# Kernel tuning notes

Hardware: AMD Instinct MI355X
Metric: run time of the kernel (lower is better)

## Reference

```python
import jax, jax.numpy as jnp
import numpy as np

B, T, C = 4, 8192, 1024
H, D = 16, 64  # n_head, head_dim


def setup_inputs() -> dict:
    key = jax.random.key(0)
    ks = jax.random.split(key, 9)
    s = 1.0 / np.sqrt(C)
    return {
        "x": jax.random.normal(ks[0], (B, T, C), jnp.float32),
        "Wq": jax.random.uniform(ks[1], (C, C), jnp.float32, -s, s),
        "bq": jax.random.uniform(ks[2], (C,), jnp.float32, -s, s),
        "Wk": jax.random.uniform(ks[3], (C, C), jnp.float32, -s, s),
        "bk": jax.random.uniform(ks[4], (C,), jnp.float32, -s, s),
        "Wv": jax.random.uniform(ks[5], (C, C), jnp.float32, -s, s),
        "bv": jax.random.uniform(ks[6], (C,), jnp.float32, -s, s),
        "Wp": jax.random.uniform(ks[7], (C, C), jnp.float32, -s, s),
        "bp": jax.random.uniform(ks[8], (C,), jnp.float32, -s, s),
    }


def _heads(t):
    # (B,T,C) -> (B,H,T,D)
    return t.reshape(B, T, H, D).transpose(0, 2, 1, 3)


def reference(x, Wq, bq, Wk, bk, Wv, bv, Wp, bp):
    q = _heads(x @ Wq.T + bq)
    k = _heads(x @ Wk.T + bk)
    v = _heads(x @ Wv.T + bv)
    # attn_type='l1': softmax q,k over feature dim; L1 normalizer
    q = jax.nn.softmax(q, axis=-1)
    k = jax.nn.softmax(k, axis=-1)
    k_sum = k.sum(axis=-2, keepdims=True)               # (B,H,1,D)
    D_inv = 1.0 / (q * k_sum).sum(axis=-1, keepdims=True)  # (B,H,T,1)
    context = jnp.einsum('bhtd,bhte->bhde', k, v)       # (B,H,D,D)
    out = jnp.einsum('bhtd,bhde->bhte', q, context) * D_inv + q
    out = out.transpose(0, 2, 1, 3).reshape(B, T, C)
    return out @ Wp.T + bp
```

## Files before the change

### kernel.cpp

```cpp
#include <hip/hip_runtime.h>
#include <hip/hip_bf16.h>
#include <stdint.h>


#define BT    32768
#define CDIM  1024

using bf16 = __hip_bfloat16;
typedef short  short8   __attribute__((ext_vector_type(8)));
typedef short  short4_t __attribute__((ext_vector_type(4)));
typedef unsigned short ushort4_t __attribute__((ext_vector_type(4)));
typedef float  floatx4  __attribute__((ext_vector_type(4)));

__device__ __forceinline__ float bfbits2f(unsigned short u) {
    union { unsigned int i; float f; } c; c.i = ((unsigned int)u) << 16; return c.f;
}

__device__ __forceinline__ void gld_lds16(const void* g, void* lds) {
    __builtin_amdgcn_global_load_lds(
        (const __attribute__((address_space(1))) uint32_t*)g,
        (__attribute__((address_space(3))) uint32_t*)lds,
        16, 0, 0);
}

__global__ void zero_kernel(float* __restrict__ p) {
    p[(size_t)blockIdx.x * 256 + threadIdx.x] = 0.0f;
}

__global__ void cvt_kernel(const float* __restrict__ x,
                           const float* __restrict__ Wq, const float* __restrict__ Wk,
                           const float* __restrict__ Wv, const float* __restrict__ Wp,
                           bf16* __restrict__ xb, bf16* __restrict__ Wb) {
    const int XF4 = (BT * CDIM) / 4;
    int i = blockIdx.x * 256 + threadIdx.x;
    const float* src; bf16* dst; int off;
    if (i < XF4) { src = x; dst = xb; off = i; }
    else {
        int i2 = i - XF4;
        int wi = i2 >> 18;
        off = i2 & 0x3FFFF;
        src = (wi == 0) ? Wq : (wi == 1) ? Wk : (wi == 2) ? Wv : Wp;
        dst = Wb + (size_t)wi * 1048576;
    }
    float4 f = ((const float4*)src)[off];
    union { bf16 h[4]; short4_t v; } u;
    u.h[0] = __float2bfloat16(f.x); u.h[1] = __float2bfloat16(f.y);
    u.h[2] = __float2bfloat16(f.z); u.h[3] = __float2bfloat16(f.w);
    *(short4_t*)(dst + (size_t)off * 4) = u.v;
}


__device__ __forceinline__ short8 frag_ld(const bf16* hb, int r, int s4q) {
    return *(const short8*)(hb + r * 64 + (((s4q) ^ (r & 7)) << 3));
}

__device__ __forceinline__ void stage_half(const bf16* g, bf16* l, int tid) {
    int ln = tid & 63, w = tid >> 6;
    int r = w * 8 + (ln >> 3);
    int c = ((ln & 7) ^ (ln >> 3)) << 3;
    gld_lds16(g + (size_t)r * CDIM + c, l + w * 512);
    gld_lds16(g + (size_t)(r + 64) * CDIM + c, l + 4096 + w * 512);
}

#define MFMA16(a, b, c) __builtin_amdgcn_mfma_f32_16x16x32_bf16(a, b, c, 0, 0, 0)
#define VMW(n) asm volatile("s_waitcnt vmcnt(" #n ")" ::: "memory")
#define VM_NONE

__device__ __forceinline__ void pipe256(const bf16* __restrict__ Ab,
                                        const bf16* __restrict__ Bb,
                                        bf16* ldsA, bf16* ldsB,
                                        int tid, floatx4 acc[8][4]) {
    const int lane = tid & 63;
    const int wv = tid >> 6;
    const int quad = lane >> 4, l15 = lane & 15;
    const int wm = wv >> 2, wn = wv & 3;
    const int rA0 = wm * 64 + l15;
    const int rB0 = (wn & 1) * 64 + l15;
    const bf16* ldsBh = ldsB + (wn >> 1) * 8192;
    short8 bfr[4][2];

#define STAGE_A(b, h, kt) stage_half(Ab + (size_t)((h) * 128) * CDIM + (kt) * 64, \
                                     ldsA + (b) * 16384 + (h) * 8192, tid)
#define STAGE_B(b, h, kt) stage_half(Bb + (size_t)((h) * 128) * CDIM + (kt) * 64, \
                                     ldsB + (b) * 16384 + (h) * 8192, tid)

#define QPHASE(BUF, QA, MM, LOADB, STG, VMC) do {                              \
    const bf16* aH_ = ldsA + (BUF) * 16384 + (QA) * 8192;                      \
    short8 a00_ = frag_ld(aH_, rA0 + (MM) * 32,      quad);                    \
    short8 a01_ = frag_ld(aH_, rA0 + (MM) * 32,      4 + quad);                \
    short8 a10_ = frag_ld(aH_, rA0 + (MM) * 32 + 16, quad);                    \
    short8 a11_ = frag_ld(aH_, rA0 + (MM) * 32 + 16, 4 + quad);                \
    if (LOADB) {                                                               \
        const bf16* bH_ = ldsBh + (BUF) * 16384;                               \
        _Pragma("unroll")                                                      \
        for (int j = 0; j < 4; ++j) {                                          \
            bfr[j][0] = frag_ld(bH_, rB0 + j * 16, quad);                      \
            bfr[j][1] = frag_ld(bH_, rB0 + j * 16, 4 + quad);                  \
        }                                                                      \
    }                                                                          \
    STG; VMC;                                                                  \
    __builtin_amdgcn_s_barrier();                                              \
    asm volatile("s_waitcnt lgkmcnt(0)" ::: "memory");                         \
    __builtin_amdgcn_s_setprio(1);                                             \
    _Pragma("unroll")                                                          \
    for (int j = 0; j < 4; ++j) {                                              \
        acc[(QA)*4+(MM)*2  ][j] = MFMA16(a00_, bfr[j][0], acc[(QA)*4+(MM)*2  ][j]); \
        acc[(QA)*4+(MM)*2  ][j] = MFMA16(a01_, bfr[j][1], acc[(QA)*4+(MM)*2  ][j]); \
        acc[(QA)*4+(MM)*2+1][j] = MFMA16(a10_, bfr[j][0], acc[(QA)*4+(MM)*2+1][j]); \
        acc[(QA)*4+(MM)*2+1][j] = MFMA16(a11_, bfr[j][1], acc[(QA)*4+(MM)*2+1][j]); \
    }                                                                          \
    __builtin_amdgcn_s_setprio(0);                                             \
    __builtin_amdgcn_s_barrier();                                              \
} while (0)

    STAGE_B(0, 0, 0); STAGE_B(0, 1, 0); STAGE_A(0, 0, 0); STAGE_A(0, 1, 0);
    STAGE_B(1, 0, 1); STAGE_B(1, 1, 1); STAGE_A(1, 0, 1);
    VMW(8);
    __builtin_amdgcn_s_barrier();

    #pragma unroll 1
    for (int i = 0; i < 7; ++i) {
        int t = 2 * i;
        QPHASE(0, 0, 0, 1, STAGE_A(1, 1, t + 1), VM_NONE);
        QPHASE(0, 0, 1, 0, STAGE_B(0, 0, t + 2), VMW(10));
        QPHASE(0, 1, 0, 0, STAGE_B(0, 1, t + 2), VM_NONE);
        QPHASE(0, 1, 1, 0, STAGE_A(0, 0, t + 2), VMW(8));
        QPHASE(1, 0, 0, 1, STAGE_A(0, 1, t + 2), VM_NONE);
        QPHASE(1, 0, 1, 0, STAGE_B(1, 0, t + 3), VMW(10));
        QPHASE(1, 1, 0, 0, STAGE_B(1, 1, t + 3), VM_NONE);
        QPHASE(1, 1, 1, 0, STAGE_A(1, 0, t + 3), VMW(8));
    }
    QPHASE(0, 0, 0, 1, STAGE_A(1, 1, 15), VM_NONE);
    QPHASE(0, 0, 1, 0, VM_NONE, VMW(8));
    QPHASE(0, 1, 0, 0, VM_NONE, VM_NONE);
    QPHASE(0, 1, 1, 0, VM_NONE, VMW(2));
    QPHASE(1, 0, 0, 1, VM_NONE, VM_NONE);
    QPHASE(1, 0, 1, 0, VM_NONE, VMW(0));
    QPHASE(1, 1, 0, 0, VM_NONE, VM_NONE);
    QPHASE(1, 1, 1, 0, VM_NONE, VM_NONE);

#undef QPHASE
#undef STAGE_A
#undef STAGE_B
}

__global__ __launch_bounds__(512, 2)
void gemm_qkv(const bf16* __restrict__ A, const bf16* __restrict__ Bw,
              const float* __restrict__ bq, const float* __restrict__ bk,
              const float* __restrict__ bv,
              bf16* __restrict__ qb, bf16* __restrict__ kb, bf16* __restrict__ vb) {
    __shared__ bf16 ldsA[32768];
    __shared__ bf16 ldsB[32768];
    int tid = threadIdx.x;
    int bid = blockIdx.x;
    int swz = (bid & 7) * 192 + (bid >> 3);
    int bn = swz % 12, bm = swz / 12;

    floatx4 acc[8][4] = {};
    pipe256(A + (size_t)bm * 256 * CDIM, Bw + (size_t)bn * 256 * CDIM,
            ldsA, ldsB, tid, acc);

    int lane = tid & 63, wv = tid >> 6, quad = lane >> 4, l15 = lane & 15;
    int wm = wv >> 2, wn = wv & 3;
    int n_abs = bn * 256 + wn * 64;
    bf16* dst; const float* biasp; int ncol0; bool smax;
    if (n_abs < 1024)      { dst = qb; biasp = bq; ncol0 = n_abs;        smax = true;  }
    else if (n_abs < 2048) { dst = kb; biasp = bk; ncol0 = n_abs - 1024; smax = true;  }
    else                   { dst = vb; biasp = bv; ncol0 = n_abs - 2048; smax = false; }
    float bias4[4];
    #pragma unroll
    for (int j = 0; j < 4; ++j) bias4[j] = biasp[ncol0 + j * 16 + l15];
    size_t row0 = (size_t)bm * 256 + wm * 64;

    #pragma unroll
    for (int i = 0; i < 8; ++i) {
        #pragma unroll
        for (int r = 0; r < 4; ++r) {
            float vals[4];
            #pragma unroll
            for (int j = 0; j < 4; ++j) vals[j] = acc[i][j][r] + bias4[j];
            if (smax) {
                float mx = fmaxf(fmaxf(vals[0], vals[1]), fmaxf(vals[2], vals[3]));
                #pragma unroll
                for (int d = 1; d < 16; d <<= 1) mx = fmaxf(mx, __shfl_xor(mx, d));
                float s = 0.f;
                #pragma unroll
                for (int j = 0; j < 4; ++j) { vals[j] = __expf(vals[j] - mx); s += vals[j]; }
                #pragma unroll
                for (int d = 1; d < 16; d <<= 1) s += __shfl_xor(s, d);
                float rinv = 1.0f / s;
                #pragma unroll
                for (int j = 0; j < 4; ++j) vals[j] *= rinv;
            }
            size_t row = row0 + ((i >> 2) * 128) + ((i & 3) * 16) + quad * 4 + r;
            #pragma unroll
            for (int j = 0; j < 4; ++j)
                dst[row * 1024 + ncol0 + j * 16 + l15] = __float2bfloat16(vals[j]);
        }
    }
}

__global__ __launch_bounds__(512, 2)
void gemm_out(const bf16* __restrict__ A, const bf16* __restrict__ Bw,
              const float* __restrict__ bp, float* __restrict__ outp) {
    __shared__ bf16 ldsA[32768];
    __shared__ bf16 ldsB[32768];
    int tid = threadIdx.x;
    int bid = blockIdx.x;
    int swz = (bid & 7) * 64 + (bid >> 3);
    int bn = swz & 3, bm = swz >> 2;

    floatx4 acc[8][4] = {};
    pipe256(A + (size_t)bm * 256 * CDIM, Bw + (size_t)bn * 256 * CDIM,
            ldsA, ldsB, tid, acc);

    int lane = tid & 63, wv = tid >> 6, quad = lane >> 4, l15 = lane & 15;
    int wm = wv >> 2, wn = wv & 3;
    int gcol0 = bn * 256 + wn * 64;
    float bias4[4];
    #pragma unroll
    for (int j = 0; j < 4; ++j) bias4[j] = bp[gcol0 + j * 16 + l15];
    size_t row0 = (size_t)bm * 256 + wm * 64;

    #pragma unroll
    for (int i = 0; i < 8; ++i) {
        #pragma unroll
        for (int r = 0; r < 4; ++r) {
            size_t row = row0 + ((i >> 2) * 128) + ((i & 3) * 16) + quad * 4 + r;
            #pragma unroll
            for (int j = 0; j < 4; ++j)
                outp[row * 1024 + gcol0 + j * 16 + l15] = acc[i][j][r] + bias4[j];
        }
    }
}

__global__ __launch_bounds__(256)
void ctx_kernel(const bf16* __restrict__ kbuf, const bf16* __restrict__ vbuf,
                float* __restrict__ ctx, float* __restrict__ ksum) {
    int bid = blockIdx.x;
    int head = bid >> 4, chunk = bid & 15;
    int b = head >> 4, h = head & 15;
    size_t rowbase = (size_t)b * 8192 + (size_t)chunk * 512;
    int coff = h * 64;
    __shared__ unsigned short kT[4096];
    __shared__ unsigned short vT[4096];
    __shared__ float ksum_s[64];
    int tid = threadIdx.x, lane = tid & 63, wv = tid >> 6;
    int quad = lane >> 4, l15 = lane & 15;
    int c8 = tid & 7, trow = tid >> 3;
    if (tid < 64) ksum_s[tid] = 0.f;

    float kacc[8] = {0.f, 0.f, 0.f, 0.f, 0.f, 0.f, 0.f, 0.f};
    floatx4 acc4[4] = {};

    size_t g0 = (rowbase + trow) * 1024 + coff + c8 * 8;
    short8 pk0 = *(const short8*)(kbuf + g0);
    short8 pk1 = *(const short8*)(kbuf + g0 + 32 * 1024);
    short8 pv0 = *(const short8*)(vbuf + g0);
    short8 pv1 = *(const short8*)(vbuf + g0 + 32 * 1024);

    int tb0 = trow >> 3;
    for (int st = 0; st < 8; ++st) {
        __syncthreads();
        #pragma unroll
        for (int j = 0; j < 8; ++j) {
            int d = c8 * 8 + j;
            int base = d * 64 + (trow & 7);
            int sw0 = (tb0 ^ j ^ c8) << 3;
            int sw1 = ((tb0 + 4) ^ j ^ c8) << 3;
            unsigned short ku0 = (unsigned short)((short*)&pk0)[j];
            unsigned short ku1 = (unsigned short)((short*)&pk1)[j];
            kT[base + sw0] = ku0;
            kT[base + sw1] = ku1;
            vT[base + sw0] = (unsigned short)((short*)&pv0)[j];
            vT[base + sw1] = (unsigned short)((short*)&pv1)[j];
            kacc[j] += bfbits2f(ku0) + bfbits2f(ku1);
        }
        __syncthreads();
        if (st < 7) {
            size_t g = g0 + (size_t)(st + 1) * 64 * 1024;
            pk0 = *(const short8*)(kbuf + g);
            pk1 = *(const short8*)(kbuf + g + 32 * 1024);
            pv0 = *(const short8*)(vbuf + g);
            pv1 = *(const short8*)(vbuf + g + 32 * 1024);
        }
        #pragma unroll
        for (int ks = 0; ks < 2; ++ks) {
            int dA = wv * 16 + l15;
            int blkA = (ks * 4 + quad) ^ (dA & 7) ^ (dA >> 3);
            short8 aF = *(const short8*)&kT[dA * 64 + (blkA << 3)];
            #pragma unroll
            for (int n = 0; n < 4; ++n) {
                int eB = n * 16 + l15;
                int blkB = (ks * 4 + quad) ^ (eB & 7) ^ (eB >> 3);
                short8 bF = *(const short8*)&vT[eB * 64 + (blkB << 3)];
                acc4[n] = MFMA16(aF, bF, acc4[n]);
            }
        }
    }

    #pragma unroll
    for (int j = 0; j < 8; ++j) {
        float v = kacc[j];
        v += __shfl_xor(v, 8); v += __shfl_xor(v, 16); v += __shfl_xor(v, 32);
        if (lane < 8) atomicAdd(&ksum_s[lane * 8 + j], v);
    }
    float* cptr = ctx + (size_t)head * 4096;
    #pragma unroll
    for (int n = 0; n < 4; ++n)
        #pragma unroll
        for (int rr = 0; rr < 4; ++rr) {
            int d = wv * 16 + quad * 4 + rr;
            int e = n * 16 + l15;
            atomicAdd(&cptr[d * 64 + e], acc4[n][rr]);
        }
    __syncthreads();
    if (tid < 64) atomicAdd(&ksum[head * 64 + tid], ksum_s[tid]);
}

#define QS 72
__global__ __launch_bounds__(256)
void attn_kernel(const bf16* __restrict__ qbuf, const float* __restrict__ ctx,
                 const float* __restrict__ ksum, bf16* __restrict__ ab) {
    int bid = blockIdx.x;
    int head = bid >> 7, tb = bid & 127;
    int b = head >> 4, h = head & 15;
    size_t row0 = (size_t)b * 8192 + (size_t)tb * 64;
    int coff = h * 64;
    __shared__ bf16 qs[64 * QS];
    __shared__ bf16 cts[64 * QS];
    __shared__ float ksums[64];
    __shared__ float dinv[64];
    int tid = threadIdx.x, lane = tid & 63, wv = tid >> 6;

    {
        int lrow = tid >> 2, lpart = tid & 3;
        size_t g = (row0 + lrow) * 1024 + coff + lpart * 16;
        short8 q0 = *(const short8*)(qbuf + g);
        short8 q1 = *(const short8*)(qbuf + g + 8);
        *(short8*)&qs[lrow * QS + lpart * 16]     = q0;
        *(short8*)&qs[lrow * QS + lpart * 16 + 8] = q1;
    }
    {
        const float* cp = ctx + (size_t)head * 4096;
        #pragma unroll
        for (int it = 0; it < 4; ++it) {
            int fi = it * 256 + tid;
            int d = fi >> 4, e0 = (fi & 15) * 4;
            float4 f = ((const float4*)cp)[fi];
            cts[(e0 + 0) * QS + d] = __float2bfloat16(f.x);
            cts[(e0 + 1) * QS + d] = __float2bfloat16(f.y);
            cts[(e0 + 2) * QS + d] = __float2bfloat16(f.z);
            cts[(e0 + 3) * QS + d] = __float2bfloat16(f.w);
        }
    }
    if (tid < 64) ksums[tid] = ksum[head * 64 + tid];
    __syncthreads();

    {
        int t = tid >> 2, dg = tid & 3;
        float p = 0.f;
        #pragma unroll
        for (int j = 0; j < 16; ++j)
            p = fmaf(__bfloat162float(qs[t * QS + dg * 16 + j]), ksums[dg * 16 + j], p);
        p += __shfl_xor(p, 1);
        p += __shfl_xor(p, 2);
        if (dg == 0) dinv[t] = 1.0f / p;
    }
    __syncthreads();

    int quad = lane >> 4, l15 = lane & 15;
    int trow0 = wv * 16;
    short8 aF0 = *(const short8*)&qs[(trow0 + l15) * QS + quad * 8];
    short8 aF1 = *(const short8*)&qs[(trow0 + l15) * QS + 32 + quad * 8];
    floatx4 acc[4] = {};
    #pragma unroll
    for (int ni = 0; ni < 4; ++ni) {
        short8 b0 = *(const short8*)&cts[(ni * 16 + l15) * QS + quad * 8];
        short8 b1 = *(const short8*)&cts[(ni * 16 + l15) * QS + 32 + quad * 8];
        acc[ni] = __builtin_amdgcn_mfma_f32_16x16x32_bf16(aF0, b0, acc[ni], 0, 0, 0);
        acc[ni] = __builtin_amdgcn_mfma_f32_16x16x32_bf16(aF1, b1, acc[ni], 0, 0, 0);
    }
    float dv[4];
    #pragma unroll
    for (int r = 0; r < 4; ++r) dv[r] = dinv[trow0 + quad * 4 + r];
    #pragma unroll
    for (int ni = 0; ni < 4; ++ni) {
        #pragma unroll
        for (int r = 0; r < 4; ++r) {
            int row = trow0 + quad * 4 + r;
            int col = ni * 16 + l15;
            float val = acc[ni][r] * dv[r] + __bfloat162float(qs[row * QS + col]);
            ab[(row0 + row) * 1024 + coff + col] = __float2bfloat16(val);
        }
    }
}

extern "C" void kernel_launch(void* const* d_in, const int* in_sizes, int n_in,
                              void* d_out, int out_size, void* d_ws, size_t ws_size,
                              hipStream_t stream) {
    const float* x  = (const float*)d_in[0];
    const float* Wq = (const float*)d_in[1];
    const float* bq = (const float*)d_in[2];
    const float* Wk = (const float*)d_in[3];
    const float* bk = (const float*)d_in[4];
    const float* Wv = (const float*)d_in[5];
    const float* bv = (const float*)d_in[6];
    const float* Wp = (const float*)d_in[7];
    const float* bp = (const float*)d_in[8];
    float* outp = (float*)d_out;

    char* ws = (char*)d_ws;
    bf16*  xb   = (bf16*)(ws);
    bf16*  Wb   = (bf16*)(ws + 67108864);
    bf16*  qb   = (bf16*)(ws + 75497472);
    bf16*  kb   = (bf16*)(ws + 142606336);
    bf16*  vb   = (bf16*)(ws + 209715200);
    float* ctx  = (float*)(ws + 276824064);
    float* ksum = (float*)(ws + 277872640);
    bf16*  ab   = (bf16*)(ws);

    zero_kernel<<<1040, 256, 0, stream>>>(ctx);
    cvt_kernel<<<36864, 256, 0, stream>>>(x, Wq, Wk, Wv, Wp, xb, Wb);
    gemm_qkv<<<1536, 512, 0, stream>>>(xb, Wb, bq, bk, bv, qb, kb, vb);
    ctx_kernel<<<1024, 256, 0, stream>>>(kb, vb, ctx, ksum);
    attn_kernel<<<8192, 256, 0, stream>>>(qb, ctx, ksum, ab);
    gemm_out<<<512, 512, 0, stream>>>(ab, Wb + (size_t)3072 * 1024, bp, outp);
}
```

Baseline: 646.7 us.

## Fuse zeroing into conversion kernel, loop attn over row tiles, nontemporal output stores

Merges the ctx/ksum zeroing kernel into the fp32→bf16 conversion kernel, which now uses a grid-stride loop with 4096 blocks instead of 36864. The attention kernel now processes four 64-row tiles per block, loading the per-head context matrix once per block and prefetching the next q tile into registers while it computes on double-buffered LDS. The output GEMM writes its final fp32 results with nontemporal stores. The aim is to cut launch count, per-block context reload and conversion work, and cache pollution from the output writes, at the cost of fewer blocks for latency hiding in the attention kernel.

```diff
diff --git a/kernel.cpp b/kernel.cpp
--- a/kernel.cpp
+++ b/kernel.cpp
@@ -23,30 +23,36 @@
         16, 0, 0);
 }
 
-__global__ void zero_kernel(float* __restrict__ p) {
-    p[(size_t)blockIdx.x * 256 + threadIdx.x] = 0.0f;
-}
-
-__global__ void cvt_kernel(const float* __restrict__ x,
-                           const float* __restrict__ Wq, const float* __restrict__ Wk,
-                           const float* __restrict__ Wv, const float* __restrict__ Wp,
-                           bf16* __restrict__ xb, bf16* __restrict__ Wb) {
+__global__ __launch_bounds__(256)
+void prep_kernel(const float* __restrict__ x,
+                 const float* __restrict__ Wq, const float* __restrict__ Wk,
+                 const float* __restrict__ Wv, const float* __restrict__ Wp,
+                 bf16* __restrict__ xb, bf16* __restrict__ Wb,
+                 float* __restrict__ zp) {
     const int XF4 = (BT * CDIM) / 4;
-    int i = blockIdx.x * 256 + threadIdx.x;
-    const float* src; bf16* dst; int off;
-    if (i < XF4) { src = x; dst = xb; off = i; }
-    else {
-        int i2 = i - XF4;
-        int wi = i2 >> 18;
-        off = i2 & 0x3FFFF;
-        src = (wi == 0) ? Wq : (wi == 1) ? Wk : (wi == 2) ? Wv : Wp;
-        dst = Wb + (size_t)wi * 1048576;
-    }
-    float4 f = ((const float4*)src)[off];
-    union { bf16 h[4]; short4_t v; } u;
-    u.h[0] = __float2bfloat16(f.x); u.h[1] = __float2bfloat16(f.y);
-    u.h[2] = __float2bfloat16(f.z); u.h[3] = __float2bfloat16(f.w);
-    *(short4_t*)(dst + (size_t)off * 4) = u.v;
+    const int TOT = XF4 + 4 * 262144;
+    int t0 = blockIdx.x * 256 + threadIdx.x;
+    if (t0 < 66560) {
+        float4 z = {0.f, 0.f, 0.f, 0.f};
+        ((float4*)zp)[t0] = z;
+    }
+    #pragma unroll 1
+    for (int i = t0; i < TOT; i += 1048576) {
+        const float* src; bf16* dst; int off;
+        if (i < XF4) { src = x; dst = xb; off = i; }
+        else {
+            int i2 = i - XF4;
+            int wi = i2 >> 18;
+            off = i2 & 0x3FFFF;
+            src = (wi == 0) ? Wq : (wi == 1) ? Wk : (wi == 2) ? Wv : Wp;
+            dst = Wb + (size_t)wi * 1048576;
+        }
+        float4 f = ((const float4*)src)[off];
+        union { bf16 h[4]; short4_t v; } u;
+        u.h[0] = __float2bfloat16(f.x); u.h[1] = __float2bfloat16(f.y);
+        u.h[2] = __float2bfloat16(f.z); u.h[3] = __float2bfloat16(f.w);
+        *(short4_t*)(dst + (size_t)off * 4) = u.v;
+    }
 }
 
 
@@ -229,7 +235,8 @@
             size_t row = row0 + ((i >> 2) * 128) + ((i & 3) * 16) + quad * 4 + r;
             #pragma unroll
             for (int j = 0; j < 4; ++j)
-                outp[row * 1024 + gcol0 + j * 16 + l15] = acc[i][j][r] + bias4[j];
+                __builtin_nontemporal_store(acc[i][j][r] + bias4[j],
+                    &outp[row * 1024 + gcol0 + j * 16 + l15]);
         }
     }
 }
@@ -323,24 +330,18 @@
 void attn_kernel(const bf16* __restrict__ qbuf, const float* __restrict__ ctx,
                  const float* __restrict__ ksum, bf16* __restrict__ ab) {
     int bid = blockIdx.x;
-    int head = bid >> 7, tb = bid & 127;
+    int head = bid >> 5, grp = bid & 31;
     int b = head >> 4, h = head & 15;
-    size_t row0 = (size_t)b * 8192 + (size_t)tb * 64;
     int coff = h * 64;
-    __shared__ bf16 qs[64 * QS];
+    __shared__ bf16 qs[2][64 * QS];
     __shared__ bf16 cts[64 * QS];
     __shared__ float ksums[64];
     __shared__ float dinv[64];
     int tid = threadIdx.x, lane = tid & 63, wv = tid >> 6;
-
-    {
-        int lrow = tid >> 2, lpart = tid & 3;
-        size_t g = (row0 + lrow) * 1024 + coff + lpart * 16;
-        short8 q0 = *(const short8*)(qbuf + g);
-        short8 q1 = *(const short8*)(qbuf + g + 8);
-        *(short8*)&qs[lrow * QS + lpart * 16]     = q0;
-        *(short8*)&qs[lrow * QS + lpart * 16 + 8] = q1;
-    }
+    int lrow = tid >> 2, lpart = tid & 3;
+    int quad = lane >> 4, l15 = lane & 15;
+    int trow0 = wv * 16;
+
     {
         const float* cp = ctx + (size_t)head * 4096;
         #pragma unroll
@@ -355,43 +356,58 @@
         }
     }
     if (tid < 64) ksums[tid] = ksum[head * 64 + tid];
-    __syncthreads();
-
-    {
-        int t = tid >> 2, dg = tid & 3;
-        float p = 0.f;
-        #pragma unroll
-        for (int j = 0; j < 16; ++j)
-            p = fmaf(__bfloat162float(qs[t * QS + dg * 16 + j]), ksums[dg * 16 + j], p);
-        p += __shfl_xor(p, 1);
-        p += __shfl_xor(p, 2);
-        if (dg == 0) dinv[t] = 1.0f / p;
-    }
-    __syncthreads();
-
-    int quad = lane >> 4, l15 = lane & 15;
-    int trow0 = wv * 16;
-    short8 aF0 = *(const short8*)&qs[(trow0 + l15) * QS + quad * 8];
-    short8 aF1 = *(const short8*)&qs[(trow0 + l15) * QS + 32 + quad * 8];
-    floatx4 acc[4] = {};
-    #pragma unroll
-    for (int ni = 0; ni < 4; ++ni) {
-        short8 b0 = *(const short8*)&cts[(ni * 16 + l15) * QS + quad * 8];
-        short8 b1 = *(const short8*)&cts[(ni * 16 + l15) * QS + 32 + quad * 8];
-        acc[ni] = __builtin_amdgcn_mfma_f32_16x16x32_bf16(aF0, b0, acc[ni], 0, 0, 0);
-        acc[ni] = __builtin_amdgcn_mfma_f32_16x16x32_bf16(aF1, b1, acc[ni], 0, 0, 0);
-    }
-    float dv[4];
-    #pragma unroll
-    for (int r = 0; r < 4; ++r) dv[r] = dinv[trow0 + quad * 4 + r];
-    #pragma unroll
-    for (int ni = 0; ni < 4; ++ni) {
-        #pragma unroll
-        for (int r = 0; r < 4; ++r) {
-            int row = trow0 + quad * 4 + r;
-            int col = ni * 16 + l15;
-            float val = acc[ni][r] * dv[r] + __bfloat162float(qs[row * QS + col]);
-            ab[(row0 + row) * 1024 + coff + col] = __float2bfloat16(val);
+
+    size_t row00 = (size_t)b * 8192 + (size_t)grp * 256;
+    size_t gq = (row00 + lrow) * 1024 + coff + lpart * 16;
+    short8 qr0 = *(const short8*)(qbuf + gq);
+    short8 qr1 = *(const short8*)(qbuf + gq + 8);
+
+    #pragma unroll 1
+    for (int it = 0; it < 4; ++it) {
+        bf16* qsb = qs[it & 1];
+        *(short8*)&qsb[lrow * QS + lpart * 16]     = qr0;
+        *(short8*)&qsb[lrow * QS + lpart * 16 + 8] = qr1;
+        __syncthreads();
+        if (it < 3) {
+            size_t g = gq + (size_t)(it + 1) * 64 * 1024;
+            qr0 = *(const short8*)(qbuf + g);
+            qr1 = *(const short8*)(qbuf + g + 8);
+        }
+        {
+            int t = tid >> 2, dg = tid & 3;
+            float p = 0.f;
+            #pragma unroll
+            for (int j = 0; j < 16; ++j)
+                p = fmaf(__bfloat162float(qsb[t * QS + dg * 16 + j]), ksums[dg * 16 + j], p);
+            p += __shfl_xor(p, 1);
+            p += __shfl_xor(p, 2);
+            if (dg == 0) dinv[t] = 1.0f / p;
+        }
+        __syncthreads();
+
+        size_t row0 = row00 + (size_t)it * 64;
+        short8 aF0 = *(const short8*)&qsb[(trow0 + l15) * QS + quad * 8];
+        short8 aF1 = *(const short8*)&qsb[(trow0 + l15) * QS + 32 + quad * 8];
+        floatx4 acc[4] = {};
+        #pragma unroll
+        for (int ni = 0; ni < 4; ++ni) {
+            short8 b0 = *(const short8*)&cts[(ni * 16 + l15) * QS + quad * 8];
+            short8 b1 = *(const short8*)&cts[(ni * 16 + l15) * QS + 32 + quad * 8];
+            acc[ni] = MFMA16(aF0, b0, acc[ni]);
+            acc[ni] = MFMA16(aF1, b1, acc[ni]);
+        }
+        float dv[4];
+        #pragma unroll
+        for (int r = 0; r < 4; ++r) dv[r] = dinv[trow0 + quad * 4 + r];
+        #pragma unroll
+        for (int ni = 0; ni < 4; ++ni) {
+            #pragma unroll
+            for (int r = 0; r < 4; ++r) {
+                int row = trow0 + quad * 4 + r;
+                int col = ni * 16 + l15;
+                float val = acc[ni][r] * dv[r] + __bfloat162float(qsb[row * QS + col]);
+                ab[(row0 + row) * 1024 + coff + col] = __float2bfloat16(val);
+            }
         }
     }
 }
@@ -420,10 +436,9 @@
     float* ksum = (float*)(ws + 277872640);
     bf16*  ab   = (bf16*)(ws);
 
-    zero_kernel<<<1040, 256, 0, stream>>>(ctx);
-    cvt_kernel<<<36864, 256, 0, stream>>>(x, Wq, Wk, Wv, Wp, xb, Wb);
+    prep_kernel<<<4096, 256, 0, stream>>>(x, Wq, Wk, Wv, Wp, xb, Wb, ctx);
     gemm_qkv<<<1536, 512, 0, stream>>>(xb, Wb, bq, bk, bv, qb, kb, vb);
     ctx_kernel<<<1024, 256, 0, stream>>>(kb, vb, ctx, ksum);
-    attn_kernel<<<8192, 256, 0, stream>>>(qb, ctx, ksum, ab);
+    attn_kernel<<<2048, 256, 0, stream>>>(qb, ctx, ksum, ab);
     gemm_out<<<512, 512, 0, stream>>>(ab, Wb + (size_t)3072 * 1024, bp, outp);
 }
```

Result: no change. 640.3 us (-1.0%).
